# Optimization experiments

Hardware: AMD Instinct MI355X
Metric: run time of the kernel (lower is better)

The kernel has to match this reference:

```python
import jax, jax.numpy as jnp
import numpy as np

HEADS = 16
EPS = 1e-6


def _rmsnorm(x, gamma):
    # x: [..., head_dim]
    inv = jax.lax.rsqrt(jnp.mean(x * x, axis=-1, keepdims=True) + EPS)
    return x * inv * gamma


def setup_inputs() -> dict:
    key = jax.random.key(0)
    ks = jax.random.split(key, 7)
    B, L, Lc, D, CTX = 4, 4096, 1024, 1024, 1024
    hd = D // HEADS
    s = 1.0 / np.sqrt(D)
    return {
        "x": jax.random.normal(ks[0], (B, L, D), jnp.float32),
        "ctx": jax.random.normal(ks[1], (B, Lc, CTX), jnp.float32),
        "Wq": jax.random.normal(ks[2], (D, D), jnp.float32) * s,
        "Wkv": jax.random.normal(ks[3], (CTX, 2 * D), jnp.float32) * s,
        "Wproj": jax.random.normal(ks[4], (D, D), jnp.float32) * s,
        "q_gamma": jnp.ones((hd,), jnp.float32),
        "k_gamma": jnp.ones((hd,), jnp.float32),
    }


def reference(x, ctx, Wq, Wkv, Wproj, q_gamma, k_gamma):
    B, L, D = x.shape
    Lc = ctx.shape[1]
    H = HEADS
    hd = D // H
    # projections
    q = (x @ Wq).reshape(B, L, H, hd).transpose(0, 2, 1, 3)        # [B,H,L,hd]
    kv = (ctx @ Wkv).reshape(B, Lc, 2, H, hd).transpose(2, 0, 3, 1, 4)
    k, v = kv[0], kv[1]                                            # [B,H,Lc,hd]
    # per-head QK RMSNorm
    q = _rmsnorm(q, q_gamma)
    k = _rmsnorm(k, k_gamma)
    scale = 1.0 / np.sqrt(hd)
    attn = jnp.einsum("bhld,bhmd->bhlm", q, k) * scale             # [B,H,L,Lc]
    attn = jax.nn.softmax(attn, axis=-1)
    out = jnp.einsum("bhlm,bhmd->bhld", attn, v)                   # [B,H,L,hd]
    out = out.transpose(0, 2, 1, 3).reshape(B, L, D)
    return out @ Wproj
```

## Files before the change

kernel.cpp:

```cpp
#include <hip/hip_runtime.h>

typedef __bf16 bf16x8 __attribute__((ext_vector_type(8)));
typedef __bf16 bf16x4 __attribute__((ext_vector_type(4)));
typedef float f32x4 __attribute__((ext_vector_type(4)));

__device__ __forceinline__ void gl_lds16(const void* g, void* l) {
  __builtin_amdgcn_global_load_lds(
      (const __attribute__((address_space(1))) unsigned int*)g,
      (__attribute__((address_space(3))) unsigned int*)l, 16, 0, 0);
}

__global__ __launch_bounds__(256) void tconv_kernel(
    const float* __restrict__ W, __bf16* __restrict__ Wt, int R, int C) {
  __shared__ float t[32][33];
  int c0 = blockIdx.x * 32, r0 = blockIdx.y * 32;
  int tx = threadIdx.x, ty = threadIdx.y;
#pragma unroll
  for (int i = 0; i < 4; ++i)
    t[ty + i * 8][tx] = W[(size_t)(r0 + ty + i * 8) * C + c0 + tx];
  __syncthreads();
#pragma unroll
  for (int i = 0; i < 4; ++i)
    Wt[(size_t)(c0 + ty + i * 8) * R + r0 + tx] = (__bf16)t[tx][ty + i * 8];
}

template <int NORM, int OUTF32, int AF32>
__global__ __launch_bounds__(256) void gemm_kernel(
    const void* __restrict__ Ain, const __bf16* __restrict__ Bt,
    void* __restrict__ Cout, void* __restrict__ Cout2,
    int M, int N, int K, const float* __restrict__ gamma) {
  __shared__ alignas(16) __bf16 Alds[2][128 * 32];
  __shared__ alignas(16) __bf16 Blds[2][128 * 32];
  const int tid = threadIdx.x;
  const int w = tid >> 6, l = tid & 63;
  const int lg = l & 15, lh = l >> 4;
  const int wr = w >> 1, wc = w & 1;

  const int nbx = gridDim.x;
  const int lid = blockIdx.y * nbx + blockIdx.x;
  const int cpx = (nbx * gridDim.y) >> 3;
  const int swz = (lid & 7) * cpx + (lid >> 3);
  const int brow = (swz / nbx) * 128, bcol = (swz % nbx) * 128;

  const __bf16* Ab = (const __bf16*)Ain;
  const float* Af = (const float*)Ain;

  const f32x4 zero = {0.f, 0.f, 0.f, 0.f};
  f32x4 acc[4][4];
#pragma unroll
  for (int m = 0; m < 4; ++m)
#pragma unroll
    for (int n = 0; n < 4; ++n) acc[m][n] = zero;

  float4 av0[2], av1[2];

  auto ALOAD = [&](int k0) {
#pragma unroll
    for (int j = 0; j < 2; ++j) {
      int c = j * 256 + w * 64 + l;
      const float* src = Af + (size_t)(brow + (c >> 2)) * K + k0 + (c & 3) * 8;
      av0[j] = ((const float4*)src)[0];
      av1[j] = ((const float4*)src)[1];
    }
  };
  auto AWRITE = [&](int buf) {
#pragma unroll
    for (int j = 0; j < 2; ++j) {
      int c = j * 256 + w * 64 + l;
      bf16x8 o;
      o[0] = (__bf16)av0[j].x; o[1] = (__bf16)av0[j].y;
      o[2] = (__bf16)av0[j].z; o[3] = (__bf16)av0[j].w;
      o[4] = (__bf16)av1[j].x; o[5] = (__bf16)av1[j].y;
      o[6] = (__bf16)av1[j].z; o[7] = (__bf16)av1[j].w;
      *(bf16x8*)((char*)Alds[buf] + c * 16) = o;
    }
  };
  auto STAGE_A16 = [&](int buf, int k0) {
#pragma unroll
    for (int j = 0; j < 2; ++j) {
      int c = j * 256 + w * 64 + l;
      gl_lds16(Ab + (size_t)(brow + (c >> 2)) * K + k0 + (c & 3) * 8,
               (char*)Alds[buf] + (j * 256 + w * 64) * 16);
    }
  };
  auto STAGE_B = [&](int buf, int k0) {
#pragma unroll
    for (int j = 0; j < 2; ++j) {
      int c = j * 256 + w * 64 + l;
      gl_lds16(Bt + (size_t)(bcol + (c >> 2)) * K + k0 + (c & 3) * 8,
               (char*)Blds[buf] + (j * 256 + w * 64) * 16);
    }
  };

  if (AF32) { ALOAD(0); STAGE_B(0, 0); AWRITE(0); }
  else      { STAGE_A16(0, 0); STAGE_B(0, 0); }
  __syncthreads();

  for (int k0 = 0; k0 < K; k0 += 32) {
    int cur = (k0 >> 5) & 1;
    const bool more = (k0 + 32 < K);
    if (more) {
      if (AF32) ALOAD(k0 + 32);
      else STAGE_A16(cur ^ 1, k0 + 32);
      STAGE_B(cur ^ 1, k0 + 32);
    }
    bf16x8 af[4], bfr[4];
#pragma unroll
    for (int m = 0; m < 4; ++m)
      af[m] = *(const bf16x8*)(Alds[cur] + (wr * 64 + m * 16 + lg) * 32 + lh * 8);
#pragma unroll
    for (int n = 0; n < 4; ++n)
      bfr[n] = *(const bf16x8*)(Blds[cur] + (wc * 64 + n * 16 + lg) * 32 + lh * 8);
#pragma unroll
    for (int m = 0; m < 4; ++m)
#pragma unroll
      for (int n = 0; n < 4; ++n)
        acc[m][n] = __builtin_amdgcn_mfma_f32_16x16x32_bf16(af[m], bfr[n], acc[m][n], 0, 0, 0);
    if (AF32 && more) AWRITE(cur ^ 1);
    __syncthreads();
  }

  const int col64 = bcol + wc * 64;
  if (NORM == 1 || (NORM == 2 && col64 < 1024)) {
    float gm[4];
#pragma unroll
    for (int n = 0; n < 4; ++n) gm[n] = gamma[n * 16 + lg];
#pragma unroll
    for (int m = 0; m < 4; ++m) {
#pragma unroll
      for (int i = 0; i < 4; ++i) {
        float ss = 0.f;
#pragma unroll
        for (int n = 0; n < 4; ++n) ss += acc[m][n][i] * acc[m][n][i];
        ss += __shfl_xor(ss, 1);
        ss += __shfl_xor(ss, 2);
        ss += __shfl_xor(ss, 4);
        ss += __shfl_xor(ss, 8);
        float inv = rsqrtf(ss * (1.0f / 64.0f) + 1e-6f);
#pragma unroll
        for (int n = 0; n < 4; ++n) acc[m][n][i] *= inv * gm[n];
      }
    }
  }

  if (NORM == 2) {
    if (col64 < 1024) {
#pragma unroll
      for (int m = 0; m < 4; ++m)
#pragma unroll
        for (int n = 0; n < 4; ++n)
#pragma unroll
          for (int i = 0; i < 4; ++i) {
            size_t idx = (size_t)(brow + wr * 64 + m * 16 + lh * 4 + i) * 1024 +
                         col64 + n * 16 + lg;
            ((__bf16*)Cout)[idx] = (__bf16)acc[m][n][i];
          }
    } else {
#pragma unroll
      for (int m = 0; m < 4; ++m) {
        int row = brow + wr * 64 + m * 16 + lh * 4;
        int bb = row >> 10, kv0 = row & 1023;
        int g = kv0 & 31;
        int pos = (kv0 & ~31) + ((g & 15) >> 2) * 8 + (g >> 4) * 4;
#pragma unroll
        for (int n = 0; n < 4; ++n) {
          int col = col64 + n * 16 + lg - 1024;
          bf16x4 v;
#pragma unroll
          for (int i = 0; i < 4; ++i) v[i] = (__bf16)acc[m][n][i];
          *(bf16x4*)((__bf16*)Cout2 + ((size_t)(bb * 1024 + col)) * 1024 + pos) = v;
        }
      }
    }
    return;
  }

#pragma unroll
  for (int m = 0; m < 4; ++m)
#pragma unroll
    for (int n = 0; n < 4; ++n)
#pragma unroll
      for (int i = 0; i < 4; ++i) {
        size_t idx = (size_t)(brow + wr * 64 + m * 16 + lh * 4 + i) * N +
                     bcol + wc * 64 + n * 16 + lg;
        if (OUTF32) ((float*)Cout)[idx] = acc[m][n][i];
        else ((__bf16*)Cout)[idx] = (__bf16)acc[m][n][i];
      }
}

__global__ __launch_bounds__(512) void flash_kernel(
    const __bf16* __restrict__ Qb, const __bf16* __restrict__ Kb,
    const __bf16* __restrict__ Vt, __bf16* __restrict__ Ob) {
  const int orig = blockIdx.x;
  const int wgid = (orig & 7) * 128 + (orig >> 3);
  const int qt = wgid & 15, h = (wgid >> 4) & 15, b = wgid >> 8;
  const int tid = threadIdx.x;
  const int w = tid >> 6, l = tid & 63, lg = l & 15, lh = l >> 4;
  __shared__ alignas(16) char lds[65536];

  const int qrow0 = b * 4096 + qt * 256 + w * 32;
  bf16x8 qfr[2][2];
#pragma unroll
  for (int mff = 0; mff < 2; ++mff)
#pragma unroll
    for (int dc = 0; dc < 2; ++dc)
      qfr[mff][dc] = *(const bf16x8*)(Qb + (size_t)(qrow0 + mff * 16 + lg) * 1024 +
                                      h * 64 + dc * 32 + lh * 8);

  const char* Kg = (const char*)Kb + (size_t)b * 2097152 + h * 128;
  const char* Vg = (const char*)Vt + (size_t)(b * 16 + h) * 64 * 2048;

  const int o16 = tid * 16;
  const int op = o16 ^ (((o16 >> 7) & 7) << 4);
  const int srow = op >> 7, scb = op & 127;

  auto STAGE = [&](int buf, int kt) {
    gl_lds16(Kg + (size_t)(kt * 64 + srow) * 2048 + scb, lds + buf * 8192 + w * 1024);
    gl_lds16(Vg + (size_t)srow * 2048 + kt * 128 + scb, lds + 32768 + buf * 8192 + w * 1024);
  };

  const int swzl = (lg & 7) << 4;
  const int off0 = lg * 128 + ((lh * 16) ^ swzl);
  const int off1 = lg * 128 + ((64 + lh * 16) ^ swzl);

  const f32x4 zero = {0.f, 0.f, 0.f, 0.f};
  f32x4 o_[4][2];
  float m_[2], lp_[2];
#pragma unroll
  for (int df = 0; df < 4; ++df)
#pragma unroll
    for (int qf = 0; qf < 2; ++qf) o_[df][qf] = zero;
  m_[0] = m_[1] = -1e30f;
  lp_[0] = lp_[1] = 0.f;

  const float C = 0.18033688f;
  const float DT = 44.361f;

  auto COMPUTE = [&](const char* Kc, const char* Vc) {
    f32x4 st[4][2];
    __builtin_amdgcn_s_setprio(1);
#pragma unroll
    for (int kvf = 0; kvf < 4; ++kvf) {
      bf16x8 kf = *(const bf16x8*)(Kc + off0 + kvf * 2048);
#pragma unroll
      for (int mff = 0; mff < 2; ++mff)
        st[kvf][mff] = __builtin_amdgcn_mfma_f32_16x16x32_bf16(kf, qfr[mff][0], zero, 0, 0, 0);
    }
#pragma unroll
    for (int kvf = 0; kvf < 4; ++kvf) {
      bf16x8 kf = *(const bf16x8*)(Kc + off1 + kvf * 2048);
#pragma unroll
      for (int mff = 0; mff < 2; ++mff)
        st[kvf][mff] = __builtin_amdgcn_mfma_f32_16x16x32_bf16(kf, qfr[mff][1], st[kvf][mff], 0, 0, 0);
    }
    __builtin_amdgcn_s_setprio(0);

    float pmax[2];
#pragma unroll
    for (int qf = 0; qf < 2; ++qf) {
      float ma[4];
#pragma unroll
      for (int i = 0; i < 4; ++i)
        ma[i] = fmaxf(fmaxf(st[0][qf][i], st[1][qf][i]),
                      fmaxf(st[2][qf][i], st[3][qf][i]));
      pmax[qf] = fmaxf(fmaxf(ma[0], ma[1]), fmaxf(ma[2], ma[3]));
    }
    int need = (pmax[0] - m_[0] > DT) || (pmax[1] - m_[1] > DT);
    if (__any(need)) {
#pragma unroll
      for (int qf = 0; qf < 2; ++qf) {
        float t = pmax[qf];
        t = fmaxf(t, __shfl_xor(t, 16));
        t = fmaxf(t, __shfl_xor(t, 32));
        float nm = fmaxf(m_[qf], t);
        float r = __builtin_amdgcn_exp2f((m_[qf] - nm) * C);
        m_[qf] = nm;
        lp_[qf] *= r;
#pragma unroll
        for (int df = 0; df < 4; ++df)
#pragma unroll
          for (int i = 0; i < 4; ++i) o_[df][qf][i] *= r;
      }
    }

    bf16x8 pw[2][2];
#pragma unroll
    for (int qf = 0; qf < 2; ++qf) {
      float rs = 0.f;
      float mc = -m_[qf] * C;
#pragma unroll
      for (int kvf = 0; kvf < 4; ++kvf) {
#pragma unroll
        for (int i = 0; i < 4; ++i) {
          float p = __builtin_amdgcn_exp2f(fmaf(st[kvf][qf][i], C, mc));
          pw[kvf >> 1][qf][(kvf & 1) * 4 + i] = (__bf16)p;
          rs += p;
        }
      }
      lp_[qf] += rs;
    }

    __builtin_amdgcn_s_setprio(1);
#pragma unroll
    for (int p = 0; p < 2; ++p)
#pragma unroll
      for (int df = 0; df < 4; ++df) {
        bf16x8 vv = *(const bf16x8*)(Vc + (p ? off1 : off0) + df * 2048);
#pragma unroll
        for (int qf = 0; qf < 2; ++qf)
          o_[df][qf] = __builtin_amdgcn_mfma_f32_16x16x32_bf16(vv, pw[p][qf], o_[df][qf], 0, 0, 0);
      }
    __builtin_amdgcn_s_setprio(0);
  };

  STAGE(0, 0);
  STAGE(1, 1);
  __syncthreads();
#pragma unroll 2
  for (int it = 0; it < 8; ++it) {
    const int pb_ = (it & 1) * 2;
    if (it < 7) {
      STAGE(pb_ ^ 2, 2 * it + 2);
      STAGE((pb_ ^ 2) + 1, 2 * it + 3);
    }
    COMPUTE(lds + pb_ * 8192, lds + 32768 + pb_ * 8192);
    COMPUTE(lds + (pb_ + 1) * 8192, lds + 32768 + (pb_ + 1) * 8192);
    asm volatile("s_waitcnt vmcnt(0)" ::: "memory");
    __syncthreads();
  }

#pragma unroll
  for (int qf = 0; qf < 2; ++qf) {
    float ls = lp_[qf];
    ls += __shfl_xor(ls, 16);
    ls += __shfl_xor(ls, 32);
    float inv = 1.f / ls;
    size_t qrow = (size_t)(qrow0 + qf * 16 + lg) * 1024 + h * 64;
#pragma unroll
    for (int df = 0; df < 4; ++df) {
      bf16x4 ov;
#pragma unroll
      for (int i = 0; i < 4; ++i) ov[i] = (__bf16)(o_[df][qf][i] * inv);
      *(bf16x4*)(Ob + qrow + df * 16 + lh * 4) = ov;
    }
  }
}

extern "C" void kernel_launch(void* const* d_in, const int* in_sizes, int n_in,
                              void* d_out, int out_size, void* d_ws, size_t ws_size,
                              hipStream_t stream) {
  const float* x     = (const float*)d_in[0];
  const float* ctx   = (const float*)d_in[1];
  const float* Wq    = (const float*)d_in[2];
  const float* Wkv   = (const float*)d_in[3];
  const float* Wproj = (const float*)d_in[4];
  const float* qg    = (const float*)d_in[5];
  const float* kg    = (const float*)d_in[6];
  float* out = (float*)d_out;

  char* ws = (char*)d_ws;
  __bf16* Ob   = (__bf16*)(ws);
  __bf16* Wqt  = (__bf16*)(ws + (size_t)40 * 1048576);
  __bf16* Wkvt = (__bf16*)(ws + (size_t)42 * 1048576);
  __bf16* Wpt  = (__bf16*)(ws + (size_t)46 * 1048576);
  __bf16* Qb   = (__bf16*)(ws + (size_t)48 * 1048576);
  __bf16* Kb   = (__bf16*)(ws + (size_t)80 * 1048576);
  __bf16* Vt   = (__bf16*)(ws + (size_t)88 * 1048576);

  tconv_kernel<<<dim3(32, 32), dim3(32, 8), 0, stream>>>(Wq, Wqt, 1024, 1024);
  tconv_kernel<<<dim3(64, 32), dim3(32, 8), 0, stream>>>(Wkv, Wkvt, 1024, 2048);
  tconv_kernel<<<dim3(32, 32), dim3(32, 8), 0, stream>>>(Wproj, Wpt, 1024, 1024);

  gemm_kernel<1, 0, 1><<<dim3(8, 128), 256, 0, stream>>>(x, Wqt, Qb, nullptr, 16384, 1024, 1024, qg);
  gemm_kernel<2, 0, 1><<<dim3(16, 32), 256, 0, stream>>>(ctx, Wkvt, Kb, Vt, 4096, 2048, 1024, kg);
  flash_kernel<<<1024, 512, 0, stream>>>(Qb, Kb, Vt, Ob);
  gemm_kernel<0, 1, 0><<<dim3(8, 128), 256, 0, stream>>>(Ob, Wpt, out, nullptr, 16384, 1024, 1024, nullptr);
}
```

Measured before the change: 262.6 us.

## Triple-buffer GEMM LDS staging with explicit waitcnt and single barrier per tile

The projection GEMM goes from double-buffered to triple-buffered LDS staging. Loads run two k-tiles ahead, and explicit s_waitcnt vmcnt counts replace the full __syncthreads, leaving one barrier per iteration. This is meant to hide global-to-LDS latency behind MFMA work and cut synchronisation stalls. It raises LDS use, which may lower occupancy, and the hand-written waitcnt counts must match the exact number of outstanding loads to stay correct.

```diff
diff --git a/kernel.cpp b/kernel.cpp
--- a/kernel.cpp
+++ b/kernel.cpp
@@ -29,8 +29,8 @@
     const void* __restrict__ Ain, const __bf16* __restrict__ Bt,
     void* __restrict__ Cout, void* __restrict__ Cout2,
     int M, int N, int K, const float* __restrict__ gamma) {
-  __shared__ alignas(16) __bf16 Alds[2][128 * 32];
-  __shared__ alignas(16) __bf16 Blds[2][128 * 32];
+  __shared__ alignas(16) __bf16 Alds[3][128 * 32];
+  __shared__ alignas(16) __bf16 Blds[3][128 * 32];
   const int tid = threadIdx.x;
   const int w = tid >> 6, l = tid & 63;
   const int lg = l & 15, lh = l >> 4;
@@ -92,18 +92,7 @@
     }
   };
 
-  if (AF32) { ALOAD(0); STAGE_B(0, 0); AWRITE(0); }
-  else      { STAGE_A16(0, 0); STAGE_B(0, 0); }
-  __syncthreads();
-
-  for (int k0 = 0; k0 < K; k0 += 32) {
-    int cur = (k0 >> 5) & 1;
-    const bool more = (k0 + 32 < K);
-    if (more) {
-      if (AF32) ALOAD(k0 + 32);
-      else STAGE_A16(cur ^ 1, k0 + 32);
-      STAGE_B(cur ^ 1, k0 + 32);
-    }
+  auto MFMA_TILE = [&](int cur) {
     bf16x8 af[4], bfr[4];
 #pragma unroll
     for (int m = 0; m < 4; ++m)
@@ -116,9 +105,43 @@
 #pragma unroll
       for (int n = 0; n < 4; ++n)
         acc[m][n] = __builtin_amdgcn_mfma_f32_16x16x32_bf16(af[m], bfr[n], acc[m][n], 0, 0, 0);
-    if (AF32 && more) AWRITE(cur ^ 1);
-    __syncthreads();
-  }
+  };
+
+  const int nt = K >> 5;
+
+  if (AF32) {
+    ALOAD(0); STAGE_B(0, 0); AWRITE(0);
+    ALOAD(32); STAGE_B(1, 32);
+  } else {
+    STAGE_A16(0, 0); STAGE_B(0, 0);
+    STAGE_A16(1, 32); STAGE_B(1, 32);
+  }
+
+  int cur = 0, nxt = 1, nx2 = 2;
+  for (int t = 0; t <= nt - 3; ++t) {
+    if (AF32) asm volatile("s_waitcnt vmcnt(6) lgkmcnt(0)" ::: "memory");
+    else      asm volatile("s_waitcnt vmcnt(4)" ::: "memory");
+    __builtin_amdgcn_s_barrier();
+    if (AF32) {
+      AWRITE(nxt);
+      ALOAD((t + 2) * 32);
+      STAGE_B(nx2, (t + 2) * 32);
+    } else {
+      STAGE_A16(nx2, (t + 2) * 32);
+      STAGE_B(nx2, (t + 2) * 32);
+    }
+    MFMA_TILE(cur);
+    int tmp = cur; cur = nxt; nxt = nx2; nx2 = tmp;
+  }
+  if (AF32) asm volatile("s_waitcnt vmcnt(6) lgkmcnt(0)" ::: "memory");
+  else      asm volatile("s_waitcnt vmcnt(4)" ::: "memory");
+  __builtin_amdgcn_s_barrier();
+  if (AF32) AWRITE(nxt);
+  MFMA_TILE(cur);
+  { int tmp = cur; cur = nxt; nxt = nx2; nx2 = tmp; }
+  asm volatile("s_waitcnt vmcnt(0) lgkmcnt(0)" ::: "memory");
+  __builtin_amdgcn_s_barrier();
+  MFMA_TILE(cur);
 
   const int col64 = bcol + wc * 64;
   if (NORM == 1 || (NORM == 2 && col64 < 1024)) {
```

Result: slower. 282.3 us (+7.5%).
